# Kernel optimization log

Measured on AMD Instinct MI355X. Metric: run time of the kernel, lower is better.

## Reference

```python
import jax, jax.numpy as jnp
import numpy as np

T, H, I, E = 512, 2048, 1408, 16
G, TOPK_GROUP, TOP_K = 4, 2, 6
RSF = 2.5  # routed_scaling_factor


def setup_inputs() -> dict:
    key = jax.random.key(0)
    ks = jax.random.split(key, 6)
    s = jnp.float32(0.02)
    return {
        "hidden_states": jax.random.normal(ks[0], (T, H), jnp.float32),
        "gate_weight": jax.random.normal(ks[1], (E, H), jnp.float32) * s,
        "correction_bias": jax.random.normal(ks[2], (E,), jnp.float32) * s,
        "w_gate": jax.random.normal(ks[3], (E, I, H), jnp.float32) * s,
        "w_up": jax.random.normal(ks[4], (E, I, H), jnp.float32) * s,
        "w_down": jax.random.normal(ks[5], (E, H, I), jnp.float32) * s,
    }


def _route(x, gate_weight, correction_bias):
    # MoEGate: logits = x @ W^T ; noaux_tc biased grouped top-k (sigmoid scoring)
    logits = x @ gate_weight.T                       # [T, E]
    scores = jax.nn.sigmoid(logits)                  # [T, E]
    sfc = scores + correction_bias                   # scores used for selection only
    # group score = sum of top-2 biased scores within each group
    gs = sfc.reshape(-1, G, E // G)                  # [T, G, E/G]
    group_scores = jax.lax.top_k(gs, 2)[0].sum(-1)   # [T, G]
    gidx = jax.lax.top_k(group_scores, TOPK_GROUP)[1]        # [T, topk_group]
    gmask = jnp.sum(jax.nn.one_hot(gidx, G, dtype=x.dtype), axis=1)  # [T, G]
    emask = jnp.repeat(gmask, E // G, axis=1)        # [T, E]
    masked = jnp.where(emask > 0, sfc, -jnp.inf)
    topk_idx = jax.lax.top_k(masked, TOP_K)[1]       # [T, K]
    # weights come from the UNbiased sigmoid scores
    topk_w = jnp.take_along_axis(scores, topk_idx, axis=1)   # [T, K]
    topk_w = topk_w / jnp.sum(topk_w, axis=-1, keepdims=True)  # renormalize
    topk_w = topk_w * jnp.asarray(RSF, x.dtype)      # routed_scaling_factor
    return topk_w, topk_idx


def _moe(x, topk_w, topk_idx, w_gate, w_up, w_down):
    # dispatch/grouped-GEMM/combine, expressed as a scan over experts with
    # per-token combine coefficients (same math as gather/grouped-GEMM/scatter)
    def step(acc, ws):
        wg, wu, wd, e = ws
        h = jax.nn.silu(x @ wg.T) * (x @ wu.T)       # [T, I] SiluAndMul
        out_e = h @ wd.T                             # [T, H]
        coef = jnp.sum(jnp.where(topk_idx == e, topk_w, 0.0), axis=1)  # [T]
        return acc + coef[:, None] * out_e, None

    acc0 = jnp.zeros_like(x)
    acc, _ = jax.lax.scan(step, acc0, (w_gate, w_up, w_down, jnp.arange(E)))
    return acc


def reference(hidden_states, gate_weight, correction_bias, w_gate, w_up, w_down):
    topk_w, topk_idx = _route(hidden_states, gate_weight, correction_bias)
    return _moe(hidden_states, topk_w, topk_idx, w_gate, w_up, w_down)
```

## Files before the change

kernel.cpp:

```cpp
#include <hip/hip_runtime.h>
#include <cstdint>

#define T_TOK 512
#define H_DIM 2048
#define I_DIM 1408
#define N_EXP 16

typedef __attribute__((ext_vector_type(8))) _Float16 f16x8;
typedef __attribute__((ext_vector_type(4))) _Float16 f16x4;
typedef __attribute__((ext_vector_type(4))) float f32x4;

__device__ __forceinline__ void gload_lds16(const void* g, void* l) {
  auto gp = (const __attribute__((address_space(1))) unsigned int*)(unsigned long long)g;
  unsigned int loff = (unsigned int)(unsigned long long)l;
  auto lp = (__attribute__((address_space(3))) unsigned int*)loff;
  __builtin_amdgcn_global_load_lds(gp, lp, 16, 0, 0);
}

__device__ __forceinline__ f16x4 cvt4(float4 v) {
  f16x4 r;
  r[0] = (_Float16)v.x; r[1] = (_Float16)v.y;
  r[2] = (_Float16)v.z; r[3] = (_Float16)v.w;
  return r;
}

__global__ __launch_bounds__(256) void route_kernel(
    const float* __restrict__ x, const float* __restrict__ gw,
    const float* __restrict__ bias, float* __restrict__ coef,
    _Float16* __restrict__ xb) {
  const int t = blockIdx.x;
  const int tid = threadIdx.x;
  const float* xt = x + (size_t)t * H_DIM;
  _Float16* xbt = xb + (size_t)t * H_DIM;

  float part[N_EXP];
#pragma unroll
  for (int e = 0; e < N_EXP; ++e) part[e] = 0.f;
  for (int j = tid; j < H_DIM; j += 256) {
    float xv = xt[j];
    xbt[j] = (_Float16)xv;
#pragma unroll
    for (int e = 0; e < N_EXP; ++e) part[e] += xv * gw[e * H_DIM + j];
  }
#pragma unroll
  for (int e = 0; e < N_EXP; ++e) {
#pragma unroll
    for (int off = 32; off > 0; off >>= 1) part[e] += __shfl_down(part[e], off);
  }
  __shared__ float red[4][N_EXP];
  const int lane = tid & 63, w = tid >> 6;
  if (lane == 0) {
#pragma unroll
    for (int e = 0; e < N_EXP; ++e) red[w][e] = part[e];
  }
  __syncthreads();
  if (tid == 0) {
    float s[16], sf[16];
    for (int e = 0; e < 16; ++e) {
      float lg = red[0][e] + red[1][e] + red[2][e] + red[3][e];
      s[e] = 1.f / (1.f + expf(-lg));
      sf[e] = s[e] + bias[e];
    }
    float gsc[4];
    for (int g = 0; g < 4; ++g) {
      float m1 = -1e30f, m2 = -1e30f;
      for (int j = 0; j < 4; ++j) {
        float v = sf[g * 4 + j];
        if (v > m1) { m2 = m1; m1 = v; }
        else if (v > m2) { m2 = v; }
      }
      gsc[g] = m1 + m2;
    }
    int g1 = 0;
    for (int g = 1; g < 4; ++g) if (gsc[g] > gsc[g1]) g1 = g;
    int g2 = -1;
    for (int g = 0; g < 4; ++g) {
      if (g == g1) continue;
      if (g2 < 0 || gsc[g] > gsc[g2]) g2 = g;
    }
    bool gok[4];
    for (int g = 0; g < 4; ++g) gok[g] = (g == g1) || (g == g2);
    bool sel[16];
    for (int e = 0; e < 16; ++e) sel[e] = false;
    float wsum = 0.f;
    for (int k = 0; k < 6; ++k) {
      int best = -1; float bv = 0.f;
      for (int e2 = 0; e2 < 16; ++e2) {
        if (!gok[e2 >> 2] || sel[e2]) continue;
        if (best < 0 || sf[e2] > bv) { bv = sf[e2]; best = e2; }
      }
      sel[best] = true;
      wsum += s[best];
    }
    float inv = 2.5f / wsum;
    for (int e = 0; e < 16; ++e) coef[t * N_EXP + e] = sel[e] ? s[e] * inv : 0.f;
  }
}

__global__ __launch_bounds__(512) void build_lists_kernel(
    const float* __restrict__ coef, int* __restrict__ counts,
    int* __restrict__ lists) {
  const int e = blockIdx.x;
  const int t = threadIdx.x;
  const bool flag = coef[t * N_EXP + e] != 0.f;
  const unsigned long long m = __ballot(flag);
  const int lane = t & 63, w = t >> 6;
  __shared__ int wcnt[8], woff[8];
  if (lane == 0) wcnt[w] = __popcll(m);
  __syncthreads();
  if (t == 0) {
    int a = 0;
    for (int i = 0; i < 8; ++i) { woff[i] = a; a += wcnt[i]; }
    counts[e] = a;
  }
  __syncthreads();
  if (flag) {
    int pos = woff[w] + __popcll(m & ((1ull << lane) - 1ull));
    lists[e * T_TOK + pos] = t;
  }
}

__global__ __launch_bounds__(256) void gate_up_kernel(
    const _Float16* __restrict__ xb, const float* __restrict__ wg,
    const float* __restrict__ wu, const int* __restrict__ counts,
    const int* __restrict__ lists, _Float16* __restrict__ hbuf) {
  const int e = blockIdx.z;
  const int ne = counts[e];
  const int row0 = blockIdx.y * 256;
  if (row0 >= ne) return;
  const int col0 = blockIdx.x * 32;
  const int tid = threadIdx.x;
  const int lane = tid & 63;
  const int w = tid >> 6;

  __shared__ _Float16 As[2][256][32];
  __shared__ _Float16 Bg[2][32][32];
  __shared__ _Float16 Bu[2][32][32];

  const int* lst = lists + e * T_TOK;
  const _Float16* asrc[4];
#pragma unroll
  for (int i = 0; i < 4; ++i) {
    int r = row0 + i * 64 + w * 16 + (lane >> 2);
    int tok = lst[min(r, ne - 1)];
    asrc[i] = xb + (size_t)tok * H_DIM + (lane & 3) * 8;
  }

  const int t2 = tid & 127;
  const int brow = t2 >> 2;
  const int bc = (t2 & 3) * 8;
  const float* bsrc = ((w < 2) ? wg : wu) +
                      ((size_t)e * I_DIM + col0 + brow) * H_DIM + bc;

  f32x4 accg[4][2], accu[4][2];
  const f32x4 zz = {0.f, 0.f, 0.f, 0.f};
#pragma unroll
  for (int m = 0; m < 4; ++m)
#pragma unroll
    for (int n = 0; n < 2; ++n) { accg[m][n] = zz; accu[m][n] = zz; }

  auto stage = [&](int kt, int buf) {
    const int k0 = kt * 32;
    float4 b0 = *(const float4*)(bsrc + k0);
    float4 b1 = *(const float4*)(bsrc + k0 + 4);
    f16x8 pb;
    pb[0] = (_Float16)b0.x; pb[1] = (_Float16)b0.y; pb[2] = (_Float16)b0.z; pb[3] = (_Float16)b0.w;
    pb[4] = (_Float16)b1.x; pb[5] = (_Float16)b1.y; pb[6] = (_Float16)b1.z; pb[7] = (_Float16)b1.w;
    _Float16* bd = (w < 2) ? &Bg[buf][brow][bc] : &Bu[buf][brow][bc];
    *(f16x8*)bd = pb;
#pragma unroll
    for (int i = 0; i < 4; ++i)
      gload_lds16(asrc[i] + k0, &As[buf][i * 64 + w * 16][0]);
  };

  auto comp = [&](int buf) {
    f16x8 afr[4], bg2[2], bu2[2];
#pragma unroll
    for (int m = 0; m < 4; ++m)
      afr[m] = *(const f16x8*)&As[buf][w * 64 + m * 16 + (lane & 15)][(lane >> 4) * 8];
#pragma unroll
    for (int n = 0; n < 2; ++n) {
      bg2[n] = *(const f16x8*)&Bg[buf][n * 16 + (lane & 15)][(lane >> 4) * 8];
      bu2[n] = *(const f16x8*)&Bu[buf][n * 16 + (lane & 15)][(lane >> 4) * 8];
    }
#pragma unroll
    for (int m = 0; m < 4; ++m)
#pragma unroll
      for (int n = 0; n < 2; ++n) {
        accg[m][n] = __builtin_amdgcn_mfma_f32_16x16x32_f16(afr[m], bg2[n], accg[m][n], 0, 0, 0);
        accu[m][n] = __builtin_amdgcn_mfma_f32_16x16x32_f16(afr[m], bu2[n], accu[m][n], 0, 0, 0);
      }
  };

  stage(0, 0);
  for (int kt = 0; kt < H_DIM / 32; ++kt) {
    __syncthreads();
    if (kt + 1 < H_DIM / 32) stage(kt + 1, (kt + 1) & 1);
    comp(kt & 1);
  }

  const int rb = w * 64 + (lane >> 4) * 4;
  const int cb = col0 + (lane & 15);
  _Float16* hb = hbuf + (size_t)e * T_TOK * I_DIM;
#pragma unroll
  for (int m = 0; m < 4; ++m) {
#pragma unroll
    for (int j = 0; j < 4; ++j) {
      int r = row0 + rb + m * 16 + j;
      if (r < ne) {
#pragma unroll
        for (int n = 0; n < 2; ++n) {
          float g = accg[m][n][j];
          float u = accu[m][n][j];
          float hv = (g / (1.f + __expf(-g))) * u;
          hb[(size_t)r * I_DIM + cb + n * 16] = (_Float16)hv;
        }
      }
    }
  }
}

__global__ __launch_bounds__(256) void down_kernel(
    const _Float16* __restrict__ hbuf, const float* __restrict__ wd,
    const int* __restrict__ counts, const int* __restrict__ lists,
    const float* __restrict__ coef, float* __restrict__ out) {
  const int e = blockIdx.z;
  const int ne = counts[e];
  const int row0 = blockIdx.y * 256;
  if (row0 >= ne) return;
  const int col0 = blockIdx.x * 32;
  const int tid = threadIdx.x;
  const int lane = tid & 63;
  const int w = tid >> 6;

  __shared__ _Float16 As[2][256][32];
  __shared__ _Float16 Bs[2][32][32];

  const _Float16* hb = hbuf + (size_t)e * T_TOK * I_DIM;
  const _Float16* asrc[4];
#pragma unroll
  for (int i = 0; i < 4; ++i) {
    int r = row0 + i * 64 + w * 16 + (lane >> 2);
    asrc[i] = hb + (size_t)r * I_DIM + (lane & 3) * 8;
  }

  const int brow = tid >> 3;
  const int bc = (tid & 7) * 4;
  const float* bsrc = wd + ((size_t)e * H_DIM + col0 + brow) * I_DIM + bc;

  f32x4 acc[4][2];
  const f32x4 zz = {0.f, 0.f, 0.f, 0.f};
#pragma unroll
  for (int m = 0; m < 4; ++m)
#pragma unroll
    for (int n = 0; n < 2; ++n) acc[m][n] = zz;

  auto stage = [&](int kt, int buf) {
    const int k0 = kt * 32;
    float4 b0 = *(const float4*)(bsrc + k0);
    *(f16x4*)&Bs[buf][brow][bc] = cvt4(b0);
#pragma unroll
    for (int i = 0; i < 4; ++i)
      gload_lds16(asrc[i] + k0, &As[buf][i * 64 + w * 16][0]);
  };

  auto comp = [&](int buf) {
    f16x8 afr[4], bfr[2];
#pragma unroll
    for (int m = 0; m < 4; ++m)
      afr[m] = *(const f16x8*)&As[buf][w * 64 + m * 16 + (lane & 15)][(lane >> 4) * 8];
#pragma unroll
    for (int n = 0; n < 2; ++n)
      bfr[n] = *(const f16x8*)&Bs[buf][n * 16 + (lane & 15)][(lane >> 4) * 8];
#pragma unroll
    for (int m = 0; m < 4; ++m)
#pragma unroll
      for (int n = 0; n < 2; ++n)
        acc[m][n] = __builtin_amdgcn_mfma_f32_16x16x32_f16(afr[m], bfr[n], acc[m][n], 0, 0, 0);
  };

  stage(0, 0);
  for (int kt = 0; kt < I_DIM / 32; ++kt) {
    __syncthreads();
    if (kt + 1 < I_DIM / 32) stage(kt + 1, (kt + 1) & 1);
    comp(kt & 1);
  }

  const int rb = w * 64 + (lane >> 4) * 4;
  const int cb = col0 + (lane & 15);
#pragma unroll
  for (int m = 0; m < 4; ++m) {
#pragma unroll
    for (int j = 0; j < 4; ++j) {
      int r = row0 + rb + m * 16 + j;
      if (r < ne) {
        int tok = lists[e * T_TOK + r];
        float c = coef[tok * N_EXP + e];
#pragma unroll
        for (int n = 0; n < 2; ++n) {
          atomicAdd(&out[(size_t)tok * H_DIM + cb + n * 16], acc[m][n][j] * c);
        }
      }
    }
  }
}

extern "C" void kernel_launch(void* const* d_in, const int* in_sizes, int n_in,
                              void* d_out, int out_size, void* d_ws, size_t ws_size,
                              hipStream_t stream) {
  const float* x  = (const float*)d_in[0];
  const float* gw = (const float*)d_in[1];
  const float* cb = (const float*)d_in[2];
  const float* wg = (const float*)d_in[3];
  const float* wu = (const float*)d_in[4];
  const float* wd = (const float*)d_in[5];
  float* out = (float*)d_out;
  char* ws = (char*)d_ws;

  float* coef   = (float*)(ws);
  int*   counts = (int*)(ws + 32768);
  int*   lists  = (int*)(ws + 33024);
  _Float16* xb  = (_Float16*)(ws + 66048);
  _Float16* hbuf= (_Float16*)(ws + 66048 + 2097152 + 256);

  hipMemsetAsync(d_out, 0, (size_t)out_size * sizeof(float), stream);

  route_kernel<<<T_TOK, 256, 0, stream>>>(x, gw, cb, coef, xb);
  build_lists_kernel<<<N_EXP, 512, 0, stream>>>(coef, counts, lists);
  gate_up_kernel<<<dim3(I_DIM / 32, 2, N_EXP), 256, 0, stream>>>(xb, wg, wu, counts, lists, hbuf);
  down_kernel<<<dim3(H_DIM / 32, 2, N_EXP), 256, 0, stream>>>(hbuf, wd, counts, lists, coef, out);
}
```

Before: 255.1 us.

## Stream fp32 weights directly to LDS with triple-buffered async pipeline

```diff
diff --git a/kernel.cpp b/kernel.cpp
--- a/kernel.cpp
+++ b/kernel.cpp
@@ -7,7 +7,6 @@
 #define N_EXP 16
 
 typedef __attribute__((ext_vector_type(8))) _Float16 f16x8;
-typedef __attribute__((ext_vector_type(4))) _Float16 f16x4;
 typedef __attribute__((ext_vector_type(4))) float f32x4;
 
 __device__ __forceinline__ void gload_lds16(const void* g, void* l) {
@@ -17,10 +16,10 @@
   __builtin_amdgcn_global_load_lds(gp, lp, 16, 0, 0);
 }
 
-__device__ __forceinline__ f16x4 cvt4(float4 v) {
-  f16x4 r;
-  r[0] = (_Float16)v.x; r[1] = (_Float16)v.y;
-  r[2] = (_Float16)v.z; r[3] = (_Float16)v.w;
+__device__ __forceinline__ f16x8 cvt8(f32x4 a, f32x4 b) {
+  f16x8 r;
+  r[0] = (_Float16)a[0]; r[1] = (_Float16)a[1]; r[2] = (_Float16)a[2]; r[3] = (_Float16)a[3];
+  r[4] = (_Float16)b[0]; r[5] = (_Float16)b[1]; r[6] = (_Float16)b[2]; r[7] = (_Float16)b[3];
   return r;
 }
 
@@ -124,6 +123,7 @@
     const _Float16* __restrict__ xb, const float* __restrict__ wg,
     const float* __restrict__ wu, const int* __restrict__ counts,
     const int* __restrict__ lists, _Float16* __restrict__ hbuf) {
+  extern __shared__ char lds[];
   const int e = blockIdx.z;
   const int ne = counts[e];
   const int row0 = blockIdx.y * 256;
@@ -133,24 +133,18 @@
   const int lane = tid & 63;
   const int w = tid >> 6;
 
-  __shared__ _Float16 As[2][256][32];
-  __shared__ _Float16 Bg[2][32][32];
-  __shared__ _Float16 Bu[2][32][32];
-
   const int* lst = lists + e * T_TOK;
   const _Float16* asrc[4];
 #pragma unroll
   for (int i = 0; i < 4; ++i) {
-    int r = row0 + i * 64 + w * 16 + (lane >> 2);
+    int r = row0 + (4 * w + i) * 16 + (lane & 15);
     int tok = lst[min(r, ne - 1)];
-    asrc[i] = xb + (size_t)tok * H_DIM + (lane & 3) * 8;
-  }
-
-  const int t2 = tid & 127;
-  const int brow = t2 >> 2;
-  const int bc = (t2 & 3) * 8;
-  const float* bsrc = ((w < 2) ? wg : wu) +
-                      ((size_t)e * I_DIM + col0 + brow) * H_DIM + bc;
+    asrc[i] = xb + (size_t)tok * H_DIM + (lane >> 4) * 8;
+  }
+  const int brow = w * 8 + (lane >> 3);
+  const int bslot = (lane & 7) ^ ((lane >> 3) & 7);
+  const float* bsg = wg + ((size_t)e * I_DIM + col0 + brow) * H_DIM + bslot * 4;
+  const float* bsu = wu + ((size_t)e * I_DIM + col0 + brow) * H_DIM + bslot * 4;
 
   f32x4 accg[4][2], accu[4][2];
   const f32x4 zz = {0.f, 0.f, 0.f, 0.f};
@@ -159,48 +153,58 @@
 #pragma unroll
     for (int n = 0; n < 2; ++n) { accg[m][n] = zz; accu[m][n] = zz; }
 
-  auto stage = [&](int kt, int buf) {
+  auto stage = [&](int kt, int b) {
     const int k0 = kt * 32;
-    float4 b0 = *(const float4*)(bsrc + k0);
-    float4 b1 = *(const float4*)(bsrc + k0 + 4);
-    f16x8 pb;
-    pb[0] = (_Float16)b0.x; pb[1] = (_Float16)b0.y; pb[2] = (_Float16)b0.z; pb[3] = (_Float16)b0.w;
-    pb[4] = (_Float16)b1.x; pb[5] = (_Float16)b1.y; pb[6] = (_Float16)b1.z; pb[7] = (_Float16)b1.w;
-    _Float16* bd = (w < 2) ? &Bg[buf][brow][bc] : &Bu[buf][brow][bc];
-    *(f16x8*)bd = pb;
 #pragma unroll
     for (int i = 0; i < 4; ++i)
-      gload_lds16(asrc[i] + k0, &As[buf][i * 64 + w * 16][0]);
+      gload_lds16(asrc[i] + k0, lds + b * 16384 + (4 * w + i) * 1024);
+    gload_lds16(bsg + k0, lds + 49152 + b * 4096 + w * 1024);
+    gload_lds16(bsu + k0, lds + 61440 + b * 4096 + w * 1024);
   };
 
-  auto comp = [&](int buf) {
-    f16x8 afr[4], bg2[2], bu2[2];
+  auto comp = [&](int b) {
+    f16x8 afr[4];
 #pragma unroll
     for (int m = 0; m < 4; ++m)
-      afr[m] = *(const f16x8*)&As[buf][w * 64 + m * 16 + (lane & 15)][(lane >> 4) * 8];
+      afr[m] = *(const f16x8*)(lds + b * 16384 + (4 * w + m) * 1024 + lane * 16);
+    const int s0 = (lane >> 4) * 2;
+    f16x8 bgf[2], buf2[2];
 #pragma unroll
     for (int n = 0; n < 2; ++n) {
-      bg2[n] = *(const f16x8*)&Bg[buf][n * 16 + (lane & 15)][(lane >> 4) * 8];
-      bu2[n] = *(const f16x8*)&Bu[buf][n * 16 + (lane & 15)][(lane >> 4) * 8];
+      const int c = n * 16 + (lane & 15);
+      const float* gp = (const float*)(lds + 49152 + b * 4096) + c * 32;
+      const float* up = (const float*)(lds + 61440 + b * 4096) + c * 32;
+      const int p0 = (s0 ^ (c & 7)) * 4;
+      const int p1 = ((s0 + 1) ^ (c & 7)) * 4;
+      bgf[n] = cvt8(*(const f32x4*)(gp + p0), *(const f32x4*)(gp + p1));
+      buf2[n] = cvt8(*(const f32x4*)(up + p0), *(const f32x4*)(up + p1));
     }
 #pragma unroll
     for (int m = 0; m < 4; ++m)
 #pragma unroll
       for (int n = 0; n < 2; ++n) {
-        accg[m][n] = __builtin_amdgcn_mfma_f32_16x16x32_f16(afr[m], bg2[n], accg[m][n], 0, 0, 0);
-        accu[m][n] = __builtin_amdgcn_mfma_f32_16x16x32_f16(afr[m], bu2[n], accu[m][n], 0, 0, 0);
+        accg[m][n] = __builtin_amdgcn_mfma_f32_16x16x32_f16(afr[m], bgf[n], accg[m][n], 0, 0, 0);
+        accu[m][n] = __builtin_amdgcn_mfma_f32_16x16x32_f16(afr[m], buf2[n], accu[m][n], 0, 0, 0);
       }
   };
 
+  const int NK = H_DIM / 32;
   stage(0, 0);
-  for (int kt = 0; kt < H_DIM / 32; ++kt) {
-    __syncthreads();
-    if (kt + 1 < H_DIM / 32) stage(kt + 1, (kt + 1) & 1);
-    comp(kt & 1);
+  stage(1, 1);
+  int cb_ = 0, sb = 2;
+  for (int kt = 0; kt < NK; ++kt) {
+    if (kt < NK - 1) { asm volatile("s_waitcnt vmcnt(6)" ::: "memory"); }
+    else             { asm volatile("s_waitcnt vmcnt(0)" ::: "memory"); }
+    __builtin_amdgcn_s_barrier();
+    __builtin_amdgcn_sched_barrier(0);
+    comp(cb_);
+    if (kt + 2 < NK) stage(kt + 2, sb);
+    cb_ = (cb_ == 2) ? 0 : cb_ + 1;
+    sb = (sb == 2) ? 0 : sb + 1;
   }
 
   const int rb = w * 64 + (lane >> 4) * 4;
-  const int cb = col0 + (lane & 15);
+  const int cbc = col0 + (lane & 15);
   _Float16* hb = hbuf + (size_t)e * T_TOK * I_DIM;
 #pragma unroll
   for (int m = 0; m < 4; ++m) {
@@ -213,7 +217,7 @@
           float g = accg[m][n][j];
           float u = accu[m][n][j];
           float hv = (g / (1.f + __expf(-g))) * u;
-          hb[(size_t)r * I_DIM + cb + n * 16] = (_Float16)hv;
+          hb[(size_t)r * I_DIM + cbc + n * 16] = (_Float16)hv;
         }
       }
     }
@@ -224,70 +228,87 @@
     const _Float16* __restrict__ hbuf, const float* __restrict__ wd,
     const int* __restrict__ counts, const int* __restrict__ lists,
     const float* __restrict__ coef, float* __restrict__ out) {
+  extern __shared__ char lds[];
   const int e = blockIdx.z;
   const int ne = counts[e];
   const int row0 = blockIdx.y * 256;
   if (row0 >= ne) return;
-  const int col0 = blockIdx.x * 32;
+  const int col0 = blockIdx.x * 64;
   const int tid = threadIdx.x;
   const int lane = tid & 63;
   const int w = tid >> 6;
 
-  __shared__ _Float16 As[2][256][32];
-  __shared__ _Float16 Bs[2][32][32];
-
   const _Float16* hb = hbuf + (size_t)e * T_TOK * I_DIM;
   const _Float16* asrc[4];
 #pragma unroll
   for (int i = 0; i < 4; ++i) {
-    int r = row0 + i * 64 + w * 16 + (lane >> 2);
-    asrc[i] = hb + (size_t)r * I_DIM + (lane & 3) * 8;
-  }
-
-  const int brow = tid >> 3;
-  const int bc = (tid & 7) * 4;
-  const float* bsrc = wd + ((size_t)e * H_DIM + col0 + brow) * I_DIM + bc;
-
-  f32x4 acc[4][2];
+    int r = row0 + (4 * w + i) * 16 + (lane & 15);
+    asrc[i] = hb + (size_t)r * I_DIM + (lane >> 4) * 8;
+  }
+  const int bslot = (lane & 7) ^ ((lane >> 3) & 7);
+  const float* bsd[2];
+#pragma unroll
+  for (int j = 0; j < 2; ++j) {
+    int brow = w * 16 + j * 8 + (lane >> 3);
+    bsd[j] = wd + ((size_t)e * H_DIM + col0 + brow) * I_DIM + bslot * 4;
+  }
+
+  f32x4 acc[4][4];
   const f32x4 zz = {0.f, 0.f, 0.f, 0.f};
 #pragma unroll
   for (int m = 0; m < 4; ++m)
 #pragma unroll
-    for (int n = 0; n < 2; ++n) acc[m][n] = zz;
-
-  auto stage = [&](int kt, int buf) {
+    for (int n = 0; n < 4; ++n) acc[m][n] = zz;
+
+  auto stage = [&](int kt, int b) {
     const int k0 = kt * 32;
-    float4 b0 = *(const float4*)(bsrc + k0);
-    *(f16x4*)&Bs[buf][brow][bc] = cvt4(b0);
 #pragma unroll
     for (int i = 0; i < 4; ++i)
-      gload_lds16(asrc[i] + k0, &As[buf][i * 64 + w * 16][0]);
+      gload_lds16(asrc[i] + k0, lds + b * 16384 + (4 * w + i) * 1024);
+#pragma unroll
+    for (int j = 0; j < 2; ++j)
+      gload_lds16(bsd[j] + k0, lds + 49152 + b * 8192 + w * 2048 + j * 1024);
   };
 
-  auto comp = [&](int buf) {
-    f16x8 afr[4], bfr[2];
+  auto comp = [&](int b) {
+    f16x8 afr[4];
 #pragma unroll
     for (int m = 0; m < 4; ++m)
-      afr[m] = *(const f16x8*)&As[buf][w * 64 + m * 16 + (lane & 15)][(lane >> 4) * 8];
-#pragma unroll
-    for (int n = 0; n < 2; ++n)
-      bfr[n] = *(const f16x8*)&Bs[buf][n * 16 + (lane & 15)][(lane >> 4) * 8];
+      afr[m] = *(const f16x8*)(lds + b * 16384 + (4 * w + m) * 1024 + lane * 16);
+    const int s0 = (lane >> 4) * 2;
+    f16x8 bdf[4];
+#pragma unroll
+    for (int n = 0; n < 4; ++n) {
+      const int c = n * 16 + (lane & 15);
+      const float* bp = (const float*)(lds + 49152 + b * 8192) + c * 32;
+      const int p0 = (s0 ^ (c & 7)) * 4;
+      const int p1 = ((s0 + 1) ^ (c & 7)) * 4;
+      bdf[n] = cvt8(*(const f32x4*)(bp + p0), *(const f32x4*)(bp + p1));
+    }
 #pragma unroll
     for (int m = 0; m < 4; ++m)
 #pragma unroll
-      for (int n = 0; n < 2; ++n)
-        acc[m][n] = __builtin_amdgcn_mfma_f32_16x16x32_f16(afr[m], bfr[n], acc[m][n], 0, 0, 0);
+      for (int n = 0; n < 4; ++n)
+        acc[m][n] = __builtin_amdgcn_mfma_f32_16x16x32_f16(afr[m], bdf[n], acc[m][n], 0, 0, 0);
   };
 
+  const int NK = I_DIM / 32;
   stage(0, 0);
-  for (int kt = 0; kt < I_DIM / 32; ++kt) {
-    __syncthreads();
-    if (kt + 1 < I_DIM / 32) stage(kt + 1, (kt + 1) & 1);
-    comp(kt & 1);
+  stage(1, 1);
+  int cb_ = 0, sb = 2;
+  for (int kt = 0; kt < NK; ++kt) {
+    if (kt < NK - 1) { asm volatile("s_waitcnt vmcnt(6)" ::: "memory"); }
+    else             { asm volatile("s_waitcnt vmcnt(0)" ::: "memory"); }
+    __builtin_amdgcn_s_barrier();
+    __builtin_amdgcn_sched_barrier(0);
+    comp(cb_);
+    if (kt + 2 < NK) stage(kt + 2, sb);
+    cb_ = (cb_ == 2) ? 0 : cb_ + 1;
+    sb = (sb == 2) ? 0 : sb + 1;
   }
 
   const int rb = w * 64 + (lane >> 4) * 4;
-  const int cb = col0 + (lane & 15);
+  const int cbc = col0 + (lane & 15);
 #pragma unroll
   for (int m = 0; m < 4; ++m) {
 #pragma unroll
@@ -297,8 +318,8 @@
         int tok = lists[e * T_TOK + r];
         float c = coef[tok * N_EXP + e];
 #pragma unroll
-        for (int n = 0; n < 2; ++n) {
-          atomicAdd(&out[(size_t)tok * H_DIM + cb + n * 16], acc[m][n][j] * c);
+        for (int n = 0; n < 4; ++n) {
+          atomicAdd(&out[(size_t)tok * H_DIM + cbc + n * 16], acc[m][n][j] * c);
         }
       }
     }
@@ -323,10 +344,15 @@
   _Float16* xb  = (_Float16*)(ws + 66048);
   _Float16* hbuf= (_Float16*)(ws + 66048 + 2097152 + 256);
 
+  hipFuncSetAttribute((const void*)gate_up_kernel,
+                      hipFuncAttributeMaxDynamicSharedMemorySize, 73728);
+  hipFuncSetAttribute((const void*)down_kernel,
+                      hipFuncAttributeMaxDynamicSharedMemorySize, 73728);
+
   hipMemsetAsync(d_out, 0, (size_t)out_size * sizeof(float), stream);
 
   route_kernel<<<T_TOK, 256, 0, stream>>>(x, gw, cb, coef, xb);
   build_lists_kernel<<<N_EXP, 512, 0, stream>>>(coef, counts, lists);
-  gate_up_kernel<<<dim3(I_DIM / 32, 2, N_EXP), 256, 0, stream>>>(xb, wg, wu, counts, lists, hbuf);
-  down_kernel<<<dim3(H_DIM / 32, 2, N_EXP), 256, 0, stream>>>(hbuf, wd, counts, lists, coef, out);
-}
+  gate_up_kernel<<<dim3(I_DIM / 32, 2, N_EXP), 256, 73728, stream>>>(xb, wg, wu, counts, lists, hbuf);
+  down_kernel<<<dim3(H_DIM / 64, 2, N_EXP), 256, 73728, stream>>>(hbuf, wd, counts, lists, coef, out);
+}
```

After: 263.9 us. +3.5%, slower.

## Replace LDS-staged block tiles with per-wave register-direct GEMM tiles

Applied to the files above, without the earlier changes.

```diff
diff --git a/kernel.cpp b/kernel.cpp
--- a/kernel.cpp
+++ b/kernel.cpp
@@ -7,20 +7,12 @@
 #define N_EXP 16
 
 typedef __attribute__((ext_vector_type(8))) _Float16 f16x8;
-typedef __attribute__((ext_vector_type(4))) _Float16 f16x4;
 typedef __attribute__((ext_vector_type(4))) float f32x4;
 
-__device__ __forceinline__ void gload_lds16(const void* g, void* l) {
-  auto gp = (const __attribute__((address_space(1))) unsigned int*)(unsigned long long)g;
-  unsigned int loff = (unsigned int)(unsigned long long)l;
-  auto lp = (__attribute__((address_space(3))) unsigned int*)loff;
-  __builtin_amdgcn_global_load_lds(gp, lp, 16, 0, 0);
-}
-
-__device__ __forceinline__ f16x4 cvt4(float4 v) {
-  f16x4 r;
-  r[0] = (_Float16)v.x; r[1] = (_Float16)v.y;
-  r[2] = (_Float16)v.z; r[3] = (_Float16)v.w;
+__device__ __forceinline__ f16x8 cvt8(f32x4 a, f32x4 b) {
+  f16x8 r;
+  r[0] = (_Float16)a[0]; r[1] = (_Float16)a[1]; r[2] = (_Float16)a[2]; r[3] = (_Float16)a[3];
+  r[4] = (_Float16)b[0]; r[5] = (_Float16)b[1]; r[6] = (_Float16)b[2]; r[7] = (_Float16)b[3];
   return r;
 }
 
@@ -120,37 +112,39 @@
   }
 }
 
-__global__ __launch_bounds__(256) void gate_up_kernel(
+__global__ __launch_bounds__(256, 2) void gate_up_kernel(
     const _Float16* __restrict__ xb, const float* __restrict__ wg,
     const float* __restrict__ wu, const int* __restrict__ counts,
     const int* __restrict__ lists, _Float16* __restrict__ hbuf) {
-  const int e = blockIdx.z;
-  const int ne = counts[e];
-  const int row0 = blockIdx.y * 256;
-  if (row0 >= ne) return;
-  const int col0 = blockIdx.x * 32;
   const int tid = threadIdx.x;
   const int lane = tid & 63;
-  const int w = tid >> 6;
-
-  __shared__ _Float16 As[2][256][32];
-  __shared__ _Float16 Bg[2][32][32];
-  __shared__ _Float16 Bu[2][32][32];
+  const int bx = blockIdx.x;
+  const int wb = (bx & 7) * 176 + (bx >> 3);
+  const int wid = wb * 4 + (tid >> 6);
+  const int rb = wid & 7;
+  const int strip = (wid >> 3) % 44;
+  const int e = wid / 352;
+  const int ne = counts[e];
+  const int row0 = rb * 64;
+  if (row0 >= ne) return;
 
   const int* lst = lists + e * T_TOK;
-  const _Float16* asrc[4];
-#pragma unroll
-  for (int i = 0; i < 4; ++i) {
-    int r = row0 + i * 64 + w * 16 + (lane >> 2);
+  const _Float16* ap[4];
+#pragma unroll
+  for (int m = 0; m < 4; ++m) {
+    int r = row0 + m * 16 + (lane & 15);
     int tok = lst[min(r, ne - 1)];
-    asrc[i] = xb + (size_t)tok * H_DIM + (lane & 3) * 8;
-  }
-
-  const int t2 = tid & 127;
-  const int brow = t2 >> 2;
-  const int bc = (t2 & 3) * 8;
-  const float* bsrc = ((w < 2) ? wg : wu) +
-                      ((size_t)e * I_DIM + col0 + brow) * H_DIM + bc;
+    ap[m] = xb + (size_t)tok * H_DIM + (lane >> 4) * 8;
+  }
+  const int col0 = strip * 32;
+  const float* gp[2];
+  const float* up[2];
+#pragma unroll
+  for (int n = 0; n < 2; ++n) {
+    size_t off = ((size_t)e * I_DIM + col0 + n * 16 + (lane & 15)) * H_DIM + (lane >> 4) * 8;
+    gp[n] = wg + off;
+    up[n] = wu + off;
+  }
 
   f32x4 accg[4][2], accu[4][2];
   const f32x4 zz = {0.f, 0.f, 0.f, 0.f};
@@ -159,94 +153,94 @@
 #pragma unroll
     for (int n = 0; n < 2; ++n) { accg[m][n] = zz; accu[m][n] = zz; }
 
-  auto stage = [&](int kt, int buf) {
-    const int k0 = kt * 32;
-    float4 b0 = *(const float4*)(bsrc + k0);
-    float4 b1 = *(const float4*)(bsrc + k0 + 4);
-    f16x8 pb;
-    pb[0] = (_Float16)b0.x; pb[1] = (_Float16)b0.y; pb[2] = (_Float16)b0.z; pb[3] = (_Float16)b0.w;
-    pb[4] = (_Float16)b1.x; pb[5] = (_Float16)b1.y; pb[6] = (_Float16)b1.z; pb[7] = (_Float16)b1.w;
-    _Float16* bd = (w < 2) ? &Bg[buf][brow][bc] : &Bu[buf][brow][bc];
-    *(f16x8*)bd = pb;
-#pragma unroll
-    for (int i = 0; i < 4; ++i)
-      gload_lds16(asrc[i] + k0, &As[buf][i * 64 + w * 16][0]);
-  };
-
-  auto comp = [&](int buf) {
-    f16x8 afr[4], bg2[2], bu2[2];
+  auto loadA = [&](f16x8 (&ab)[4], int k0) {
+#pragma unroll
+    for (int m = 0; m < 4; ++m) ab[m] = *(const f16x8*)(ap[m] + k0);
+  };
+  auto loadB = [&](f32x4 (&gb)[2][2], f32x4 (&ub)[2][2], int k0) {
+#pragma unroll
+    for (int n = 0; n < 2; ++n) {
+      gb[n][0] = *(const f32x4*)(gp[n] + k0);
+      gb[n][1] = *(const f32x4*)(gp[n] + k0 + 4);
+      ub[n][0] = *(const f32x4*)(up[n] + k0);
+      ub[n][1] = *(const f32x4*)(up[n] + k0 + 4);
+    }
+  };
+  auto compute = [&](f16x8 (&ab)[4], f32x4 (&gb)[2][2], f32x4 (&ub)[2][2]) {
+    f16x8 bg[2], bu[2];
+#pragma unroll
+    for (int n = 0; n < 2; ++n) {
+      bg[n] = cvt8(gb[n][0], gb[n][1]);
+      bu[n] = cvt8(ub[n][0], ub[n][1]);
+    }
 #pragma unroll
     for (int m = 0; m < 4; ++m)
-      afr[m] = *(const f16x8*)&As[buf][w * 64 + m * 16 + (lane & 15)][(lane >> 4) * 8];
-#pragma unroll
-    for (int n = 0; n < 2; ++n) {
-      bg2[n] = *(const f16x8*)&Bg[buf][n * 16 + (lane & 15)][(lane >> 4) * 8];
-      bu2[n] = *(const f16x8*)&Bu[buf][n * 16 + (lane & 15)][(lane >> 4) * 8];
-    }
-#pragma unroll
-    for (int m = 0; m < 4; ++m)
 #pragma unroll
       for (int n = 0; n < 2; ++n) {
-        accg[m][n] = __builtin_amdgcn_mfma_f32_16x16x32_f16(afr[m], bg2[n], accg[m][n], 0, 0, 0);
-        accu[m][n] = __builtin_amdgcn_mfma_f32_16x16x32_f16(afr[m], bu2[n], accu[m][n], 0, 0, 0);
-      }
-  };
-
-  stage(0, 0);
-  for (int kt = 0; kt < H_DIM / 32; ++kt) {
-    __syncthreads();
-    if (kt + 1 < H_DIM / 32) stage(kt + 1, (kt + 1) & 1);
-    comp(kt & 1);
-  }
-
-  const int rb = w * 64 + (lane >> 4) * 4;
-  const int cb = col0 + (lane & 15);
+        accg[m][n] = __builtin_amdgcn_mfma_f32_16x16x32_f16(ab[m], bg[n], accg[m][n], 0, 0, 0);
+        accu[m][n] = __builtin_amdgcn_mfma_f32_16x16x32_f16(ab[m], bu[n], accu[m][n], 0, 0, 0);
+      }
+  };
+
+  f16x8 a0[4], a1[4];
+  f32x4 g0[2][2], u0[2][2], g1[2][2], u1[2][2];
+  loadA(a0, 0); loadB(g0, u0, 0);
+  for (int kt = 0; kt < H_DIM / 32; kt += 2) {
+    loadA(a1, (kt + 1) * 32); loadB(g1, u1, (kt + 1) * 32);
+    compute(a0, g0, u0);
+    if (kt + 2 < H_DIM / 32) { loadA(a0, (kt + 2) * 32); loadB(g0, u0, (kt + 2) * 32); }
+    compute(a1, g1, u1);
+  }
+
+  const int rr = (lane >> 4) * 4;
+  const int cc = col0 + (lane & 15);
   _Float16* hb = hbuf + (size_t)e * T_TOK * I_DIM;
 #pragma unroll
   for (int m = 0; m < 4; ++m) {
 #pragma unroll
     for (int j = 0; j < 4; ++j) {
-      int r = row0 + rb + m * 16 + j;
+      int r = row0 + m * 16 + rr + j;
       if (r < ne) {
 #pragma unroll
         for (int n = 0; n < 2; ++n) {
           float g = accg[m][n][j];
           float u = accu[m][n][j];
           float hv = (g / (1.f + __expf(-g))) * u;
-          hb[(size_t)r * I_DIM + cb + n * 16] = (_Float16)hv;
+          hb[(size_t)r * I_DIM + cc + n * 16] = (_Float16)hv;
         }
       }
     }
   }
 }
 
-__global__ __launch_bounds__(256) void down_kernel(
+__global__ __launch_bounds__(256, 3) void down_kernel(
     const _Float16* __restrict__ hbuf, const float* __restrict__ wd,
     const int* __restrict__ counts, const int* __restrict__ lists,
     const float* __restrict__ coef, float* __restrict__ out) {
-  const int e = blockIdx.z;
-  const int ne = counts[e];
-  const int row0 = blockIdx.y * 256;
-  if (row0 >= ne) return;
-  const int col0 = blockIdx.x * 32;
   const int tid = threadIdx.x;
   const int lane = tid & 63;
-  const int w = tid >> 6;
-
-  __shared__ _Float16 As[2][256][32];
-  __shared__ _Float16 Bs[2][32][32];
+  const int bx = blockIdx.x;
+  const int wb = (bx & 7) * 256 + (bx >> 3);
+  const int wid = wb * 4 + (tid >> 6);
+  const int rb = wid & 7;
+  const int cs = (wid >> 3) & 63;
+  const int e = wid >> 9;
+  const int ne = counts[e];
+  const int row0 = rb * 64;
+  if (row0 >= ne) return;
 
   const _Float16* hb = hbuf + (size_t)e * T_TOK * I_DIM;
-  const _Float16* asrc[4];
-#pragma unroll
-  for (int i = 0; i < 4; ++i) {
-    int r = row0 + i * 64 + w * 16 + (lane >> 2);
-    asrc[i] = hb + (size_t)r * I_DIM + (lane & 3) * 8;
-  }
-
-  const int brow = tid >> 3;
-  const int bc = (tid & 7) * 4;
-  const float* bsrc = wd + ((size_t)e * H_DIM + col0 + brow) * I_DIM + bc;
+  const _Float16* ap[4];
+#pragma unroll
+  for (int m = 0; m < 4; ++m) {
+    int r = row0 + m * 16 + (lane & 15);
+    ap[m] = hb + (size_t)r * I_DIM + (lane >> 4) * 8;
+  }
+  const int col0 = cs * 32;
+  const float* bp[2];
+#pragma unroll
+  for (int n = 0; n < 2; ++n)
+    bp[n] = wd + ((size_t)e * H_DIM + col0 + n * 16 + (lane & 15)) * I_DIM + (lane >> 4) * 8;
 
   f32x4 acc[4][2];
   const f32x4 zz = {0.f, 0.f, 0.f, 0.f};
@@ -255,51 +249,51 @@
 #pragma unroll
     for (int n = 0; n < 2; ++n) acc[m][n] = zz;
 
-  auto stage = [&](int kt, int buf) {
-    const int k0 = kt * 32;
-    float4 b0 = *(const float4*)(bsrc + k0);
-    *(f16x4*)&Bs[buf][brow][bc] = cvt4(b0);
-#pragma unroll
-    for (int i = 0; i < 4; ++i)
-      gload_lds16(asrc[i] + k0, &As[buf][i * 64 + w * 16][0]);
-  };
-
-  auto comp = [&](int buf) {
-    f16x8 afr[4], bfr[2];
+  auto loadA = [&](f16x8 (&ab)[4], int k0) {
+#pragma unroll
+    for (int m = 0; m < 4; ++m) ab[m] = *(const f16x8*)(ap[m] + k0);
+  };
+  auto loadB = [&](f32x4 (&bb)[2][2], int k0) {
+#pragma unroll
+    for (int n = 0; n < 2; ++n) {
+      bb[n][0] = *(const f32x4*)(bp[n] + k0);
+      bb[n][1] = *(const f32x4*)(bp[n] + k0 + 4);
+    }
+  };
+  auto compute = [&](f16x8 (&ab)[4], f32x4 (&bb)[2][2]) {
+    f16x8 bf[2];
+#pragma unroll
+    for (int n = 0; n < 2; ++n) bf[n] = cvt8(bb[n][0], bb[n][1]);
 #pragma unroll
     for (int m = 0; m < 4; ++m)
-      afr[m] = *(const f16x8*)&As[buf][w * 64 + m * 16 + (lane & 15)][(lane >> 4) * 8];
-#pragma unroll
-    for (int n = 0; n < 2; ++n)
-      bfr[n] = *(const f16x8*)&Bs[buf][n * 16 + (lane & 15)][(lane >> 4) * 8];
-#pragma unroll
-    for (int m = 0; m < 4; ++m)
 #pragma unroll
       for (int n = 0; n < 2; ++n)
-        acc[m][n] = __builtin_amdgcn_mfma_f32_16x16x32_f16(afr[m], bfr[n], acc[m][n], 0, 0, 0);
-  };
-
-  stage(0, 0);
-  for (int kt = 0; kt < I_DIM / 32; ++kt) {
-    __syncthreads();
-    if (kt + 1 < I_DIM / 32) stage(kt + 1, (kt + 1) & 1);
-    comp(kt & 1);
-  }
-
-  const int rb = w * 64 + (lane >> 4) * 4;
-  const int cb = col0 + (lane & 15);
+        acc[m][n] = __builtin_amdgcn_mfma_f32_16x16x32_f16(ab[m], bf[n], acc[m][n], 0, 0, 0);
+  };
+
+  f16x8 a0[4], a1[4];
+  f32x4 b0[2][2], b1[2][2];
+  loadA(a0, 0); loadB(b0, 0);
+  for (int kt = 0; kt < I_DIM / 32; kt += 2) {
+    loadA(a1, (kt + 1) * 32); loadB(b1, (kt + 1) * 32);
+    compute(a0, b0);
+    if (kt + 2 < I_DIM / 32) { loadA(a0, (kt + 2) * 32); loadB(b0, (kt + 2) * 32); }
+    compute(a1, b1);
+  }
+
+  const int rr = (lane >> 4) * 4;
+  const int cc = col0 + (lane & 15);
 #pragma unroll
   for (int m = 0; m < 4; ++m) {
 #pragma unroll
     for (int j = 0; j < 4; ++j) {
-      int r = row0 + rb + m * 16 + j;
+      int r = row0 + m * 16 + rr + j;
       if (r < ne) {
         int tok = lists[e * T_TOK + r];
         float c = coef[tok * N_EXP + e];
 #pragma unroll
-        for (int n = 0; n < 2; ++n) {
-          atomicAdd(&out[(size_t)tok * H_DIM + cb + n * 16], acc[m][n][j] * c);
-        }
+        for (int n = 0; n < 2; ++n)
+          atomicAdd(&out[(size_t)tok * H_DIM + cc + n * 16], acc[m][n][j] * c);
       }
     }
   }
@@ -327,6 +321,6 @@
 
   route_kernel<<<T_TOK, 256, 0, stream>>>(x, gw, cb, coef, xb);
   build_lists_kernel<<<N_EXP, 512, 0, stream>>>(coef, counts, lists);
-  gate_up_kernel<<<dim3(I_DIM / 32, 2, N_EXP), 256, 0, stream>>>(xb, wg, wu, counts, lists, hbuf);
-  down_kernel<<<dim3(H_DIM / 32, 2, N_EXP), 256, 0, stream>>>(hbuf, wd, counts, lists, coef, out);
-}
+  gate_up_kernel<<<1408, 256, 0, stream>>>(xb, wg, wu, counts, lists, hbuf);
+  down_kernel<<<2048, 256, 0, stream>>>(hbuf, wd, counts, lists, coef, out);
+}
```

After: 866.0 us. +239.5%, slower.

## Enlarge GEMM tiles, async-load fp32 weights into swizzled LDS, convert at fragment load

Applied to the files above, without the earlier changes.

```diff
diff --git a/kernel.cpp b/kernel.cpp
--- a/kernel.cpp
+++ b/kernel.cpp
@@ -7,7 +7,6 @@
 #define N_EXP 16
 
 typedef __attribute__((ext_vector_type(8))) _Float16 f16x8;
-typedef __attribute__((ext_vector_type(4))) _Float16 f16x4;
 typedef __attribute__((ext_vector_type(4))) float f32x4;
 
 __device__ __forceinline__ void gload_lds16(const void* g, void* l) {
@@ -17,10 +16,10 @@
   __builtin_amdgcn_global_load_lds(gp, lp, 16, 0, 0);
 }
 
-__device__ __forceinline__ f16x4 cvt4(float4 v) {
-  f16x4 r;
-  r[0] = (_Float16)v.x; r[1] = (_Float16)v.y;
-  r[2] = (_Float16)v.z; r[3] = (_Float16)v.w;
+__device__ __forceinline__ f16x8 cvt8(f32x4 a, f32x4 b) {
+  f16x8 r;
+  r[0] = (_Float16)a[0]; r[1] = (_Float16)a[1]; r[2] = (_Float16)a[2]; r[3] = (_Float16)a[3];
+  r[4] = (_Float16)b[0]; r[5] = (_Float16)b[1]; r[6] = (_Float16)b[2]; r[7] = (_Float16)b[3];
   return r;
 }
 
@@ -120,37 +119,39 @@
   }
 }
 
-__global__ __launch_bounds__(256) void gate_up_kernel(
+__global__ __launch_bounds__(512) void gate_up_kernel(
     const _Float16* __restrict__ xb, const float* __restrict__ wg,
     const float* __restrict__ wu, const int* __restrict__ counts,
     const int* __restrict__ lists, _Float16* __restrict__ hbuf) {
+  extern __shared__ char lds[];
   const int e = blockIdx.z;
   const int ne = counts[e];
   const int row0 = blockIdx.y * 256;
   if (row0 >= ne) return;
-  const int col0 = blockIdx.x * 32;
+  const int col0 = blockIdx.x * 64;
   const int tid = threadIdx.x;
   const int lane = tid & 63;
   const int w = tid >> 6;
-
-  __shared__ _Float16 As[2][256][32];
-  __shared__ _Float16 Bg[2][32][32];
-  __shared__ _Float16 Bu[2][32][32];
+  const int wr = w >> 1, wc = w & 1;
 
   const int* lst = lists + e * T_TOK;
   const _Float16* asrc[4];
 #pragma unroll
   for (int i = 0; i < 4; ++i) {
-    int r = row0 + i * 64 + w * 16 + (lane >> 2);
-    int tok = lst[min(r, ne - 1)];
-    asrc[i] = xb + (size_t)tok * H_DIM + (lane & 3) * 8;
-  }
-
-  const int t2 = tid & 127;
-  const int brow = t2 >> 2;
-  const int bc = (t2 & 3) * 8;
-  const float* bsrc = ((w < 2) ? wg : wu) +
-                      ((size_t)e * I_DIM + col0 + brow) * H_DIM + bc;
+    int tr = (w * 4 + i) * 8 + (lane >> 3);
+    int tok = lst[min(row0 + tr, ne - 1)];
+    int lchunk = (lane & 7) ^ (tr & 7);
+    asrc[i] = xb + (size_t)tok * H_DIM + lchunk * 8;
+  }
+  const float* bgs[2];
+  const float* bus[2];
+#pragma unroll
+  for (int i = 0; i < 2; ++i) {
+    int tr = (w * 2 + i) * 4 + (lane >> 4);
+    int ls = (lane & 15) ^ ((tr & 7) << 1);
+    bgs[i] = wg + ((size_t)e * I_DIM + col0 + tr) * H_DIM + ls * 4;
+    bus[i] = wu + ((size_t)e * I_DIM + col0 + tr) * H_DIM + ls * 4;
+  }
 
   f32x4 accg[4][2], accu[4][2];
   const f32x4 zz = {0.f, 0.f, 0.f, 0.f};
@@ -160,93 +161,109 @@
     for (int n = 0; n < 2; ++n) { accg[m][n] = zz; accu[m][n] = zz; }
 
   auto stage = [&](int kt, int buf) {
-    const int k0 = kt * 32;
-    float4 b0 = *(const float4*)(bsrc + k0);
-    float4 b1 = *(const float4*)(bsrc + k0 + 4);
-    f16x8 pb;
-    pb[0] = (_Float16)b0.x; pb[1] = (_Float16)b0.y; pb[2] = (_Float16)b0.z; pb[3] = (_Float16)b0.w;
-    pb[4] = (_Float16)b1.x; pb[5] = (_Float16)b1.y; pb[6] = (_Float16)b1.z; pb[7] = (_Float16)b1.w;
-    _Float16* bd = (w < 2) ? &Bg[buf][brow][bc] : &Bu[buf][brow][bc];
-    *(f16x8*)bd = pb;
+    const int k0 = kt * 64;
 #pragma unroll
     for (int i = 0; i < 4; ++i)
-      gload_lds16(asrc[i] + k0, &As[buf][i * 64 + w * 16][0]);
+      gload_lds16(asrc[i] + k0, lds + buf * 32768 + (w * 4 + i) * 1024);
+#pragma unroll
+    for (int i = 0; i < 2; ++i) {
+      gload_lds16(bgs[i] + k0, lds + 65536 + buf * 16384 + (w * 2 + i) * 1024);
+      gload_lds16(bus[i] + k0, lds + 98304 + buf * 16384 + (w * 2 + i) * 1024);
+    }
   };
 
   auto comp = [&](int buf) {
-    f16x8 afr[4], bg2[2], bu2[2];
-#pragma unroll
-    for (int m = 0; m < 4; ++m)
-      afr[m] = *(const f16x8*)&As[buf][w * 64 + m * 16 + (lane & 15)][(lane >> 4) * 8];
-#pragma unroll
-    for (int n = 0; n < 2; ++n) {
-      bg2[n] = *(const f16x8*)&Bg[buf][n * 16 + (lane & 15)][(lane >> 4) * 8];
-      bu2[n] = *(const f16x8*)&Bu[buf][n * 16 + (lane & 15)][(lane >> 4) * 8];
-    }
-#pragma unroll
-    for (int m = 0; m < 4; ++m)
+    const char* Ab = lds + buf * 32768;
+    const char* Gb = lds + 65536 + buf * 16384;
+    const char* Ub = lds + 98304 + buf * 16384;
+#pragma unroll
+    for (int kk = 0; kk < 2; ++kk) {
+      f16x8 afr[4], bg[2], bu[2];
+#pragma unroll
+      for (int m = 0; m < 4; ++m) {
+        int row = wr * 64 + m * 16 + (lane & 15);
+        int pch = (kk * 4 + (lane >> 4)) ^ (row & 7);
+        afr[m] = *(const f16x8*)(Ab + row * 128 + pch * 16);
+      }
 #pragma unroll
       for (int n = 0; n < 2; ++n) {
-        accg[m][n] = __builtin_amdgcn_mfma_f32_16x16x32_f16(afr[m], bg2[n], accg[m][n], 0, 0, 0);
-        accu[m][n] = __builtin_amdgcn_mfma_f32_16x16x32_f16(afr[m], bu2[n], accu[m][n], 0, 0, 0);
-      }
+        int c = wc * 32 + n * 16 + (lane & 15);
+        int s0 = kk * 8 + (lane >> 4) * 2;
+        int p0 = s0 ^ ((c & 7) << 1);
+        int p1 = (s0 + 1) ^ ((c & 7) << 1);
+        bg[n] = cvt8(*(const f32x4*)(Gb + c * 256 + p0 * 16),
+                     *(const f32x4*)(Gb + c * 256 + p1 * 16));
+        bu[n] = cvt8(*(const f32x4*)(Ub + c * 256 + p0 * 16),
+                     *(const f32x4*)(Ub + c * 256 + p1 * 16));
+      }
+#pragma unroll
+      for (int m = 0; m < 4; ++m)
+#pragma unroll
+        for (int n = 0; n < 2; ++n) {
+          accg[m][n] = __builtin_amdgcn_mfma_f32_16x16x32_f16(afr[m], bg[n], accg[m][n], 0, 0, 0);
+          accu[m][n] = __builtin_amdgcn_mfma_f32_16x16x32_f16(afr[m], bu[n], accu[m][n], 0, 0, 0);
+        }
+    }
   };
 
+  const int NK = H_DIM / 64;
   stage(0, 0);
-  for (int kt = 0; kt < H_DIM / 32; ++kt) {
+  for (int kt = 0; kt < NK; ++kt) {
     __syncthreads();
-    if (kt + 1 < H_DIM / 32) stage(kt + 1, (kt + 1) & 1);
+    if (kt + 1 < NK) stage(kt + 1, (kt + 1) & 1);
     comp(kt & 1);
   }
 
-  const int rb = w * 64 + (lane >> 4) * 4;
-  const int cb = col0 + (lane & 15);
   _Float16* hb = hbuf + (size_t)e * T_TOK * I_DIM;
 #pragma unroll
   for (int m = 0; m < 4; ++m) {
 #pragma unroll
     for (int j = 0; j < 4; ++j) {
-      int r = row0 + rb + m * 16 + j;
+      int r = row0 + wr * 64 + m * 16 + (lane >> 4) * 4 + j;
       if (r < ne) {
 #pragma unroll
         for (int n = 0; n < 2; ++n) {
+          int cc = col0 + wc * 32 + n * 16 + (lane & 15);
           float g = accg[m][n][j];
           float u = accu[m][n][j];
           float hv = (g / (1.f + __expf(-g))) * u;
-          hb[(size_t)r * I_DIM + cb + n * 16] = (_Float16)hv;
+          hb[(size_t)r * I_DIM + cc] = (_Float16)hv;
         }
       }
     }
   }
 }
 
-__global__ __launch_bounds__(256) void down_kernel(
+__global__ __launch_bounds__(512) void down_kernel(
     const _Float16* __restrict__ hbuf, const float* __restrict__ wd,
     const int* __restrict__ counts, const int* __restrict__ lists,
     const float* __restrict__ coef, float* __restrict__ out) {
+  extern __shared__ char lds[];
   const int e = blockIdx.z;
   const int ne = counts[e];
   const int row0 = blockIdx.y * 256;
   if (row0 >= ne) return;
-  const int col0 = blockIdx.x * 32;
+  const int col0 = blockIdx.x * 64;
   const int tid = threadIdx.x;
   const int lane = tid & 63;
   const int w = tid >> 6;
-
-  __shared__ _Float16 As[2][256][32];
-  __shared__ _Float16 Bs[2][32][32];
+  const int wr = w >> 1, wc = w & 1;
 
   const _Float16* hb = hbuf + (size_t)e * T_TOK * I_DIM;
   const _Float16* asrc[4];
 #pragma unroll
   for (int i = 0; i < 4; ++i) {
-    int r = row0 + i * 64 + w * 16 + (lane >> 2);
-    asrc[i] = hb + (size_t)r * I_DIM + (lane & 3) * 8;
-  }
-
-  const int brow = tid >> 3;
-  const int bc = (tid & 7) * 4;
-  const float* bsrc = wd + ((size_t)e * H_DIM + col0 + brow) * I_DIM + bc;
+    int tr = (w * 4 + i) * 8 + (lane >> 3);
+    int lchunk = (lane & 7) ^ (tr & 7);
+    asrc[i] = hb + (size_t)(row0 + tr) * I_DIM + lchunk * 8;
+  }
+  const float* bds[2];
+#pragma unroll
+  for (int i = 0; i < 2; ++i) {
+    int tr = (w * 2 + i) * 4 + (lane >> 4);
+    int ls = (lane & 15) ^ ((tr & 7) << 1);
+    bds[i] = wd + ((size_t)e * H_DIM + col0 + tr) * I_DIM + ls * 4;
+  }
 
   f32x4 acc[4][2];
   const f32x4 zz = {0.f, 0.f, 0.f, 0.f};
@@ -256,49 +273,64 @@
     for (int n = 0; n < 2; ++n) acc[m][n] = zz;
 
   auto stage = [&](int kt, int buf) {
-    const int k0 = kt * 32;
-    float4 b0 = *(const float4*)(bsrc + k0);
-    *(f16x4*)&Bs[buf][brow][bc] = cvt4(b0);
+    const int k0 = kt * 64;
 #pragma unroll
     for (int i = 0; i < 4; ++i)
-      gload_lds16(asrc[i] + k0, &As[buf][i * 64 + w * 16][0]);
+      gload_lds16(asrc[i] + k0, lds + buf * 32768 + (w * 4 + i) * 1024);
+#pragma unroll
+    for (int i = 0; i < 2; ++i)
+      gload_lds16(bds[i] + k0, lds + 65536 + buf * 16384 + (w * 2 + i) * 1024);
   };
 
   auto comp = [&](int buf) {
-    f16x8 afr[4], bfr[2];
-#pragma unroll
-    for (int m = 0; m < 4; ++m)
-      afr[m] = *(const f16x8*)&As[buf][w * 64 + m * 16 + (lane & 15)][(lane >> 4) * 8];
-#pragma unroll
-    for (int n = 0; n < 2; ++n)
-      bfr[n] = *(const f16x8*)&Bs[buf][n * 16 + (lane & 15)][(lane >> 4) * 8];
-#pragma unroll
-    for (int m = 0; m < 4; ++m)
-#pragma unroll
-      for (int n = 0; n < 2; ++n)
-        acc[m][n] = __builtin_amdgcn_mfma_f32_16x16x32_f16(afr[m], bfr[n], acc[m][n], 0, 0, 0);
+    const char* Ab = lds + buf * 32768;
+    const char* Bb = lds + 65536 + buf * 16384;
+#pragma unroll
+    for (int kk = 0; kk < 2; ++kk) {
+      f16x8 afr[4], bf[2];
+#pragma unroll
+      for (int m = 0; m < 4; ++m) {
+        int row = wr * 64 + m * 16 + (lane & 15);
+        int pch = (kk * 4 + (lane >> 4)) ^ (row & 7);
+        afr[m] = *(const f16x8*)(Ab + row * 128 + pch * 16);
+      }
+#pragma unroll
+      for (int n = 0; n < 2; ++n) {
+        int c = wc * 32 + n * 16 + (lane & 15);
+        int s0 = kk * 8 + (lane >> 4) * 2;
+        int p0 = s0 ^ ((c & 7) << 1);
+        int p1 = (s0 + 1) ^ ((c & 7) << 1);
+        bf[n] = cvt8(*(const f32x4*)(Bb + c * 256 + p0 * 16),
+                     *(const f32x4*)(Bb + c * 256 + p1 * 16));
+      }
+#pragma unroll
+      for (int m = 0; m < 4; ++m)
+#pragma unroll
+        for (int n = 0; n < 2; ++n)
+          acc[m][n] = __builtin_amdgcn_mfma_f32_16x16x32_f16(afr[m], bf[n], acc[m][n], 0, 0, 0);
+    }
   };
 
+  const int NK = I_DIM / 64;
   stage(0, 0);
-  for (int kt = 0; kt < I_DIM / 32; ++kt) {
+  for (int kt = 0; kt < NK; ++kt) {
     __syncthreads();
-    if (kt + 1 < I_DIM / 32) stage(kt + 1, (kt + 1) & 1);
+    if (kt + 1 < NK) stage(kt + 1, (kt + 1) & 1);
     comp(kt & 1);
   }
 
-  const int rb = w * 64 + (lane >> 4) * 4;
-  const int cb = col0 + (lane & 15);
 #pragma unroll
   for (int m = 0; m < 4; ++m) {
 #pragma unroll
     for (int j = 0; j < 4; ++j) {
-      int r = row0 + rb + m * 16 + j;
+      int r = row0 + wr * 64 + m * 16 + (lane >> 4) * 4 + j;
       if (r < ne) {
         int tok = lists[e * T_TOK + r];
         float c = coef[tok * N_EXP + e];
 #pragma unroll
         for (int n = 0; n < 2; ++n) {
-          atomicAdd(&out[(size_t)tok * H_DIM + cb + n * 16], acc[m][n][j] * c);
+          int cc = col0 + wc * 32 + n * 16 + (lane & 15);
+          atomicAdd(&out[(size_t)tok * H_DIM + cc], acc[m][n][j] * c);
         }
       }
     }
@@ -323,10 +355,15 @@
   _Float16* xb  = (_Float16*)(ws + 66048);
   _Float16* hbuf= (_Float16*)(ws + 66048 + 2097152 + 256);
 
+  hipFuncSetAttribute((const void*)gate_up_kernel,
+                      hipFuncAttributeMaxDynamicSharedMemorySize, 131072);
+  hipFuncSetAttribute((const void*)down_kernel,
+                      hipFuncAttributeMaxDynamicSharedMemorySize, 98304);
+
   hipMemsetAsync(d_out, 0, (size_t)out_size * sizeof(float), stream);
 
   route_kernel<<<T_TOK, 256, 0, stream>>>(x, gw, cb, coef, xb);
   build_lists_kernel<<<N_EXP, 512, 0, stream>>>(coef, counts, lists);
-  gate_up_kernel<<<dim3(I_DIM / 32, 2, N_EXP), 256, 0, stream>>>(xb, wg, wu, counts, lists, hbuf);
-  down_kernel<<<dim3(H_DIM / 32, 2, N_EXP), 256, 0, stream>>>(hbuf, wd, counts, lists, coef, out);
-}
+  gate_up_kernel<<<dim3(I_DIM / 64, 2, N_EXP), 512, 131072, stream>>>(xb, wg, wu, counts, lists, hbuf);
+  down_kernel<<<dim3(H_DIM / 64, 2, N_EXP), 512, 98304, stream>>>(hbuf, wd, counts, lists, coef, out);
+}
```

After: 213.1 us. -16.5%, faster.
